# Kernel tuning notes

Measured on AMD Instinct MI355X. Metric: run time of the kernel, lower is better.

The kernel has to match this reference:

```python
import jax, jax.numpy as jnp
import numpy as np

KNB = 64  # max_num_neighbors in torch_geometric radius query


def fps(p, n):
    # Farthest point sampling, deterministic start at index 0. p: [N,3] -> [n] int32
    N = p.shape[0]
    def step(carry, _):
        d, last = carry
        d = jnp.minimum(d, jnp.sum((p - p[last]) ** 2, -1))
        return (d, jnp.argmax(d).astype(jnp.int32)), last
    _, idx = jax.lax.scan(step, (jnp.full((N,), jnp.inf, p.dtype), jnp.int32(0)), None, length=n)
    return idx


def mlp3(h, w1, b1, w2, b2, w3, b3):
    # torch_geometric-style MLP: Lin+ReLU per layer (batch_norm disabled)
    h = jax.nn.relu(h @ w1 + b1)
    h = jax.nn.relu(h @ w2 + b2)
    return jax.nn.relu(h @ w3 + b3)


def sa_module(x, pos, S, r, params):
    # PointNet++ set abstraction: FPS -> ball query -> per-edge MLP -> max pool.
    # x: [B,N,C], pos: [B,N,3] -> ([B,S,Cout], [B,S,3])
    B, N, _ = pos.shape
    idx = jax.vmap(lambda p: fps(p, S))(pos)                           # [B,S]
    ctr = jnp.take_along_axis(pos, idx[:, :, None], 1)                 # [B,S,3]
    d2 = jnp.sum((ctr[:, :, None, :] - pos[:, None, :, :]) ** 2, -1)   # [B,S,N]
    mask = d2 <= r * r
    # first KNB in-radius points in index order (emulates radius() neighbor cap)
    score = jnp.where(mask, (N - jnp.arange(N, dtype=jnp.int32))[None, None, :], 0)
    vals, nb = jax.lax.top_k(score, KNB)                               # [B,S,KNB]
    valid = vals > 0
    flat = nb.reshape(B, S * KNB)
    xj = jnp.take_along_axis(x, flat[:, :, None], 1).reshape(B, S, KNB, -1)
    pj = jnp.take_along_axis(pos, flat[:, :, None], 1).reshape(B, S, KNB, 3)
    feat = jnp.concatenate([xj, pj - ctr[:, :, None, :]], -1)          # [B,S,KNB,C+3]
    h = mlp3(feat, *params)
    h = jnp.where(valid[..., None], h, -jnp.inf)
    return h.max(axis=2), ctr                                          # max-aggr over ball


def setup_inputs() -> dict:
    key = jax.random.key(0)
    ks = jax.random.split(key, 64)
    inp = {}
    inp["x"] = jax.random.normal(ks[0], (16, 2048, 9), jnp.float32)
    inp["pos"] = jax.random.uniform(ks[1], (16, 2048, 3), dtype=jnp.float32)
    i = 2
    for tag, c0, c1, c2, c3 in [("s1", 12, 64, 64, 128), ("s2", 131, 128, 128, 256),
                                 ("s3", 259, 256, 512, 1024), ("f", 1024, 512, 512, 256)]:
        for j, (ci, co) in enumerate([(c0, c1), (c1, c2), (c2, c3)], 1):
            inp[f"{tag}w{j}"] = jax.random.normal(ks[i], (ci, co), jnp.float32) / np.sqrt(ci); i += 1
            inp[f"{tag}b{j}"] = jnp.zeros((co,), jnp.float32)
    for j, (ci, co) in enumerate([(1024, 512), (512, 256), (256, 256), (256, 128), (128, 128)], 1):
        inp[f"l{j}w"] = jax.random.normal(ks[i], (ci, co), jnp.float32) / np.sqrt(ci); i += 1
        inp[f"l{j}b"] = jnp.zeros((co,), jnp.float32)
    return inp


def reference(x, pos,
              s1w1, s1b1, s1w2, s1b2, s1w3, s1b3,
              s2w1, s2b1, s2w2, s2b2, s2w3, s2b3,
              s3w1, s3b1, s3w2, s3b2, s3w3, s3b3,
              fw1, fb1, fw2, fb2, fw3, fb3,
              l1w, l1b, l2w, l2b, l3w, l3b, l4w, l4b, l5w, l5b):
    KP1 = 4  # K+1 frames per sample; B = n_batch*(K+1)
    x1, p1 = sa_module(x, pos, 1024, 0.2, (s1w1, s1b1, s1w2, s1b2, s1w3, s1b3))
    x2, p2 = sa_module(x1, p1, 256, 0.4, (s2w1, s2b1, s2w2, s2b2, s2w3, s2b3))
    # GlobalSAModule: MLP then global max pool over remaining points
    g = mlp3(jnp.concatenate([x2, p2], -1), s3w1, s3b1, s3w2, s3b2, s3w3, s3b3).max(axis=1)  # [B,1024]
    h = jax.nn.relu(g @ l1w + l1b)
    h = jax.nn.relu(h @ l2w + l2b)
    h = h @ l3w + l3b                       # [B,256]
    h = h.reshape(-1, KP1 * 256)            # [n_batch, 1024]
    h = mlp3(h, fw1, fb1, fw2, fb2, fw3, fb3)  # fusion_type == 0
    h = jax.nn.relu(h @ l4w + l4b)
    return h @ l5w + l5b                    # [n_batch, z_dim=128]
```

## Files before the change

kernel.cpp:

```cpp
#include <hip/hip_runtime.h>
#include <cstddef>

#define DEVINF __builtin_inff()

typedef __attribute__((ext_vector_type(8))) short bf16x8;
typedef __attribute__((ext_vector_type(4))) float f32x4;
typedef __attribute__((ext_vector_type(2))) float f32x2;

__device__ __forceinline__ unsigned short f2bf(float x) {
  unsigned u = __float_as_uint(x);
  return (unsigned short)((u + 0x7fff + ((u >> 16) & 1)) >> 16);
}
__device__ __forceinline__ float bf2f(unsigned short h) {
  return __uint_as_float(((unsigned)h) << 16);
}
__device__ __forceinline__ void split_bf(float x, unsigned short& hi, unsigned short& lo) {
  hi = f2bf(x);
  lo = f2bf(x - bf2f(hi));
}

#define FPS_RED_LEVEL(CTRL)                                                      \
  {                                                                              \
    int th = __builtin_amdgcn_update_dpp((int)hi, (int)hi, CTRL, 0xf, 0xf, false); \
    int tl = __builtin_amdgcn_update_dpp((int)lo, (int)lo, CTRL, 0xf, 0xf, false); \
    bool take = ((unsigned)th > hi) || (((unsigned)th == hi) && ((unsigned)tl > lo)); \
    hi = take ? (unsigned)th : hi;                                               \
    lo = take ? (unsigned)tl : lo;                                               \
  }

template <int PPLH, int NCH>
__device__ __forceinline__ unsigned long long fps_wave_step(
    f32x2* qx, f32x2* qy, f32x2* qz, f32x2* d, float lx, float ly, float lz,
    int lane, int ibase) {
#pragma clang fp contract(off)
  const int CH = PPLH / NCH;
  float bv[NCH];
  int bi[NCH];
#pragma unroll
  for (int c = 0; c < NCH; ++c) { bv[c] = -DEVINF; bi[c] = 0x7fffffff; }
  f32x2 lxv = {lx, lx}, lyv = {ly, ly}, lzv = {lz, lz};
#pragma unroll
  for (int h = 0; h < PPLH; ++h) {
    const int c = h / CH;
    f32x2 dx = qx[h] - lxv, dy = qy[h] - lyv, dz = qz[h] - lzv;
    f32x2 t0 = dx * dx, t1 = dy * dy, t2 = dz * dz;
    f32x2 d2 = (t0 + t1) + t2;
    f32x2 dn;
    dn.x = fminf(d[h].x, d2.x);
    dn.y = fminf(d[h].y, d2.y);
    d[h] = dn;
    int i0 = ibase + (2 * h) * 64 + lane;
    if (dn.x > bv[c]) { bv[c] = dn.x; bi[c] = i0; }
    if (dn.y > bv[c]) { bv[c] = dn.y; bi[c] = i0 + 64; }
  }
  unsigned hi, lo;
  if (NCH == 4) {
    unsigned h0 = __float_as_uint(bv[0]), l0 = ~(unsigned)bi[0];
    unsigned h1 = __float_as_uint(bv[1]), l1 = ~(unsigned)bi[1];
    unsigned h2 = __float_as_uint(bv[2]), l2 = ~(unsigned)bi[2];
    unsigned h3 = __float_as_uint(bv[3]), l3 = ~(unsigned)bi[3];
    bool t01 = (h1 > h0) || ((h1 == h0) && (l1 > l0));
    unsigned ha = t01 ? h1 : h0, la = t01 ? l1 : l0;
    bool t23 = (h3 > h2) || ((h3 == h2) && (l3 > l2));
    unsigned hb = t23 ? h3 : h2, lb = t23 ? l3 : l2;
    bool tab = (hb > ha) || ((hb == ha) && (lb > la));
    hi = tab ? hb : ha;
    lo = tab ? lb : la;
  } else {
    const int c1 = (NCH > 1) ? 1 : 0;
    unsigned h0 = __float_as_uint(bv[0]), l0 = ~(unsigned)bi[0];
    unsigned h1 = __float_as_uint(bv[c1]), l1 = ~(unsigned)bi[c1];
    bool t01 = (h1 > h0) || ((h1 == h0) && (l1 > l0));
    hi = t01 ? h1 : h0;
    lo = t01 ? l1 : l0;
  }
  FPS_RED_LEVEL(0x111)
  FPS_RED_LEVEL(0x112)
  FPS_RED_LEVEL(0x114)
  FPS_RED_LEVEL(0x118)
  FPS_RED_LEVEL(0x142)
  FPS_RED_LEVEL(0x143)
  return (((unsigned long long)hi) << 32) | lo;
}

struct PrepJobs {
  const float* src[9];
  unsigned short* hi[9];
  unsigned short* lo[9];
  int K[9], N[9], rl[9];
  int blk0[10];
};

__global__ __launch_bounds__(256, 1) void fps1_prep_kernel(
    const float* __restrict__ pos, float* __restrict__ p1, PrepJobs jb) {
#pragma clang fp contract(off)
  const int tid = threadIdx.x;
  if (blockIdx.x >= 16) {
    int blk = blockIdx.x - 16;
    int j = 0;
#pragma unroll
    for (int t = 1; t < 9; ++t)
      if (blk >= jb.blk0[t]) j = t;
    int idx = (blk - jb.blk0[j]) * 256 + tid;
    int rl = jb.rl[j], N = jb.N[j], K = jb.K[j];
    if (idx >= N * rl) return;
    int n = idx / rl, k = idx - n * rl;
    float v = (k < K) ? jb.src[j][(size_t)k * N + n] : 0.f;
    unsigned short h, l;
    split_bf(v, h, l);
    jb.hi[j][idx] = h;
    jb.lo[j][idx] = l;
    return;
  }
  const int b = blockIdx.x;
  const int w = tid >> 6, lane = tid & 63;
  __shared__ __align__(16) float4 p4[2048];
  __shared__ __align__(16) float4 carr[1024];
  __shared__ unsigned long long kv[2][4];
  f32x2 qx[4], qy[4], qz[4], d[4];
  const int ibase = w * 512;
#pragma unroll
  for (int h = 0; h < 4; ++h) {
    int i0 = ibase + (2 * h) * 64 + lane, i1 = i0 + 64;
    const float* a = pos + ((size_t)b * 2048 + i0) * 3;
    const float* c = pos + ((size_t)b * 2048 + i1) * 3;
    float x0 = a[0], y0 = a[1], z0 = a[2];
    float x1 = c[0], y1 = c[1], z1 = c[2];
    qx[h].x = x0; qx[h].y = x1;
    qy[h].x = y0; qy[h].y = y1;
    qz[h].x = z0; qz[h].y = z1;
    d[h].x = DEVINF; d[h].y = DEVINF;
    p4[i0] = float4{x0, y0, z0, 0.f};
    p4[i1] = float4{x1, y1, z1, 0.f};
  }
  __syncthreads();
  int last = 0;
  for (int s = 0; s < 1024; ++s) {
    float4 c4 = p4[last];
    if (tid == 0) carr[s] = c4;
    unsigned long long k =
        fps_wave_step<4, 4>(qx, qy, qz, d, c4.x, c4.y, c4.z, lane, ibase);
    if (lane == 63) kv[s & 1][w] = k;
    __syncthreads();
    unsigned long long k0 = kv[s & 1][0], k1 = kv[s & 1][1];
    unsigned long long k2 = kv[s & 1][2], k3 = kv[s & 1][3];
    unsigned long long ka = k0 > k1 ? k0 : k1;
    unsigned long long kb = k2 > k3 ? k2 : k3;
    unsigned long long kk = ka > kb ? ka : kb;
    last = (int)~(unsigned)kk;
  }
  for (int i = tid; i < 1024; i += 256) {
    float4 c = carr[i];
    p1[((size_t)b * 1024 + i) * 3 + 0] = c.x;
    p1[((size_t)b * 1024 + i) * 3 + 1] = c.y;
    p1[((size_t)b * 1024 + i) * 3 + 2] = c.z;
  }
}

template <int KS, int T>
__device__ __forceinline__ void mfma_allm(
    const unsigned short* __restrict__ inHi, const unsigned short* __restrict__ inLo,
    int sIn, const unsigned short* __restrict__ wHi,
    const unsigned short* __restrict__ wLo, int rl, const float* __restrict__ bias,
    int n0, int lane, f32x4 acc[4][T]) {
  const int col = lane & 15, quad = lane >> 4;
#pragma unroll
  for (int t = 0; t < T; ++t) {
    float bv = bias[n0 + t * 16 + col];
#pragma unroll
    for (int mt = 0; mt < 4; ++mt) {
      acc[mt][t].x = bv; acc[mt][t].y = bv; acc[mt][t].z = bv; acc[mt][t].w = bv;
    }
  }
  size_t b0 = (size_t)(n0 + col) * rl + quad * 8;
  bf16x8 bh = *(const bf16x8*)(wHi + b0);
  bf16x8 bl = *(const bf16x8*)(wLo + b0);
#pragma unroll 1
  for (int ks = 0; ks < KS; ++ks) {
    bf16x8 ah[4], al[4];
#pragma unroll
    for (int mt = 0; mt < 4; ++mt) {
      int aoff = (mt * 16 + col) * sIn + ks * 32 + quad * 8;
      ah[mt] = *(const bf16x8*)(inHi + aoff);
      al[mt] = *(const bf16x8*)(inLo + aoff);
    }
#pragma unroll
    for (int t = 0; t < T; ++t) {
      int nks = (t + 1 < T) ? ks : ks + 1;
      int nt = (t + 1 < T) ? t + 1 : 0;
      if (nks > KS - 1) nks = KS - 1;
      size_t nboff = (size_t)(n0 + nt * 16 + col) * rl + nks * 32 + quad * 8;
      bf16x8 nh = *(const bf16x8*)(wHi + nboff);
      bf16x8 nl = *(const bf16x8*)(wLo + nboff);
#pragma unroll
      for (int mt = 0; mt < 4; ++mt) {
        acc[mt][t] = __builtin_amdgcn_mfma_f32_16x16x32_bf16(ah[mt], bh, acc[mt][t], 0, 0, 0);
        acc[mt][t] = __builtin_amdgcn_mfma_f32_16x16x32_bf16(ah[mt], bl, acc[mt][t], 0, 0, 0);
        acc[mt][t] = __builtin_amdgcn_mfma_f32_16x16x32_bf16(al[mt], bh, acc[mt][t], 0, 0, 0);
      }
      bh = nh;
      bl = nl;
    }
  }
}

template <int T>
__device__ __forceinline__ void store_allm(const f32x4 acc[4][T], int n0,
                                           unsigned short* outHi,
                                           unsigned short* outLo, int sOut,
                                           int lane) {
  const int col = lane & 15, quad = lane >> 4;
#pragma unroll
  for (int mt = 0; mt < 4; ++mt)
#pragma unroll
    for (int t = 0; t < T; ++t)
#pragma unroll
      for (int r = 0; r < 4; ++r) {
        int edge = mt * 16 + quad * 4 + r;
        float v = fmaxf(acc[mt][t][r], 0.f);
        unsigned short h, l;
        split_bf(v, h, l);
        outHi[edge * sOut + n0 + t * 16 + col] = h;
        outLo[edge * sOut + n0 + t * 16 + col] = l;
      }
}

template <int T>
__device__ __forceinline__ void outpool_allm(const f32x4 acc[4][T], int n0,
                                             float* __restrict__ outp, int nvalid,
                                             int lane) {
  const int col = lane & 15, quad = lane >> 4;
#pragma unroll
  for (int t = 0; t < T; ++t) {
    float m = -DEVINF;
#pragma unroll
    for (int mt = 0; mt < 4; ++mt)
#pragma unroll
      for (int r = 0; r < 4; ++r) {
        int edge = mt * 16 + quad * 4 + r;
        float v = fmaxf(acc[mt][t][r], 0.f);
        if (edge >= nvalid) v = -DEVINF;
        m = fmaxf(m, v);
      }
    m = fmaxf(m, __shfl_xor(m, 16, 64));
    m = fmaxf(m, __shfl_xor(m, 32, 64));
    if (quad == 0) outp[n0 + t * 16 + col] = m;
  }
}

template <int KS, int T>
__device__ __forceinline__ void mfma_1m(
    const unsigned short* __restrict__ inHi, const unsigned short* __restrict__ inLo,
    int sIn, const unsigned short* __restrict__ wHi,
    const unsigned short* __restrict__ wLo, int rl, const float* __restrict__ bias,
    int n0, int lane, f32x4 acc[T]) {
  const int col = lane & 15, quad = lane >> 4;
#pragma unroll
  for (int t = 0; t < T; ++t) {
    float bv = bias[n0 + t * 16 + col];
    acc[t].x = bv; acc[t].y = bv; acc[t].z = bv; acc[t].w = bv;
  }
  size_t b0 = (size_t)(n0 + col) * rl + quad * 8;
  bf16x8 bh = *(const bf16x8*)(wHi + b0);
  bf16x8 bl = *(const bf16x8*)(wLo + b0);
#pragma unroll 1
  for (int ks = 0; ks < KS; ++ks) {
    int aoff = col * sIn + ks * 32 + quad * 8;
    bf16x8 ah = *(const bf16x8*)(inHi + aoff);
    bf16x8 al = *(const bf16x8*)(inLo + aoff);
#pragma unroll
    for (int t = 0; t < T; ++t) {
      int nks = (t + 1 < T) ? ks : ks + 1;
      int nt = (t + 1 < T) ? t + 1 : 0;
      if (nks > KS - 1) nks = KS - 1;
      size_t nboff = (size_t)(n0 + nt * 16 + col) * rl + nks * 32 + quad * 8;
      bf16x8 nh = *(const bf16x8*)(wHi + nboff);
      bf16x8 nl = *(const bf16x8*)(wLo + nboff);
      acc[t] = __builtin_amdgcn_mfma_f32_16x16x32_bf16(ah, bh, acc[t], 0, 0, 0);
      acc[t] = __builtin_amdgcn_mfma_f32_16x16x32_bf16(ah, bl, acc[t], 0, 0, 0);
      acc[t] = __builtin_amdgcn_mfma_f32_16x16x32_bf16(al, bh, acc[t], 0, 0, 0);
      bh = nh;
      bl = nl;
    }
  }
}

template <int T>
__device__ __forceinline__ void store_1m(const f32x4 acc[T], int n0,
                                         unsigned short* outHi,
                                         unsigned short* outLo, int sOut, int lane) {
  const int col = lane & 15, quad = lane >> 4;
#pragma unroll
  for (int t = 0; t < T; ++t)
#pragma unroll
    for (int r = 0; r < 4; ++r) {
      int p = quad * 4 + r;
      float v = fmaxf(acc[t][r], 0.f);
      unsigned short h, l;
      split_bf(v, h, l);
      outHi[p * sOut + n0 + t * 16 + col] = h;
      outLo[p * sOut + n0 + t * 16 + col] = l;
    }
}

__global__ __launch_bounds__(256, 4) void sa1_kernel(
    const float* __restrict__ x,
    const float* __restrict__ pos,
    const float* __restrict__ ctr,
    float* __restrict__ p2,
    const unsigned short* __restrict__ w1h, const unsigned short* __restrict__ w1l,
    const unsigned short* __restrict__ w2h, const unsigned short* __restrict__ w2l,
    const unsigned short* __restrict__ w3h, const unsigned short* __restrict__ w3l,
    const float* __restrict__ b1, const float* __restrict__ b2,
    const float* __restrict__ b3,
    float* __restrict__ out)
{
  const int N = 2048;
  const float r2 = (float)(0.2 * 0.2);
  const int tid = threadIdx.x;
  const int w = tid >> 6, lane = tid & 63;
  __shared__ __align__(16) unsigned short smem[4 * 4608];
  unsigned short* bufA_hi = smem;
  unsigned short* bufA_lo = smem + 4608;
  unsigned short* bufB_hi = smem + 9216;
  unsigned short* bufB_lo = smem + 13824;
  __shared__ int nb[64];
  __shared__ int tot[4];
  __shared__ unsigned long long kv2[2][4];

  if (blockIdx.x < 16) {
    const int bb = blockIdx.x;
    float4* q4 = (float4*)smem;
    float4* carr = (float4*)(smem + 8192);
    for (int i = tid; i < 1024; i += 256) {
      const float* pr = ctr + ((size_t)bb * 1024 + i) * 3;
      q4[i] = float4{pr[0], pr[1], pr[2], 0.f};
    }
    __syncthreads();
    f32x2 qx[2], qy[2], qz[2], d[2];
    const int ibase = w * 256;
#pragma unroll
    for (int h = 0; h < 2; ++h) {
      int i0 = ibase + (2 * h) * 64 + lane, i1 = i0 + 64;
      float4 a = q4[i0], c = q4[i1];
      qx[h].x = a.x; qx[h].y = c.x;
      qy[h].x = a.y; qy[h].y = c.y;
      qz[h].x = a.z; qz[h].y = c.z;
      d[h].x = DEVINF; d[h].y = DEVINF;
    }
    int last = 0;
    for (int s = 0; s < 256; ++s) {
      float4 c4 = q4[last];
      if (tid == 0) carr[s] = c4;
      unsigned long long k =
          fps_wave_step<2, 2>(qx, qy, qz, d, c4.x, c4.y, c4.z, lane, ibase);
      if (lane == 63) kv2[s & 1][w] = k;
      __syncthreads();
      unsigned long long k0 = kv2[s & 1][0], k1 = kv2[s & 1][1];
      unsigned long long k2 = kv2[s & 1][2], k3 = kv2[s & 1][3];
      unsigned long long ka = k0 > k1 ? k0 : k1;
      unsigned long long kb = k2 > k3 ? k2 : k3;
      unsigned long long kk = ka > kb ? ka : kb;
      last = (int)~(unsigned)kk;
    }
    {
      float4 c = carr[tid];
      if (tid < 256) {
        p2[((size_t)bb * 256 + tid) * 3 + 0] = c.x;
        p2[((size_t)bb * 256 + tid) * 3 + 1] = c.y;
        p2[((size_t)bb * 256 + tid) * 3 + 2] = c.z;
      }
    }
    return;
  }

  const int bs = blockIdx.x - 16;
  const int b = bs >> 10;
  const float cx = ctr[bs * 3 + 0], cy = ctr[bs * 3 + 1], cz = ctr[bs * 3 + 2];
  nb[lane] = 0;
  unsigned long long mloc[8];
  {
#pragma clang fp contract(off)
#pragma unroll
    for (int it = 0; it < 8; ++it) {
      int i = (w * 8 + it) * 64 + lane;
      const float* p = pos + ((size_t)b * N + i) * 3;
      float dx = p[0] - cx, dy = p[1] - cy, dz = p[2] - cz;
      float t0 = dx * dx, t1 = dy * dy, t2 = dz * dz;
      float d2 = (t0 + t1) + t2;
      mloc[it] = __ballot(d2 <= r2);
    }
  }
  {
    int mytot = 0;
#pragma unroll
    for (int it = 0; it < 8; ++it) mytot += (int)__popcll(mloc[it]);
    if (lane == 0) tot[w] = mytot;
  }
  __syncthreads();
  const int t0s = tot[0], t1s = tot[1], t2s = tot[2], t3s = tot[3];
  {
    int cnt = (w > 0 ? t0s : 0) + (w > 1 ? t1s : 0) + (w > 2 ? t2s : 0);
#pragma unroll
    for (int it = 0; it < 8; ++it) {
      unsigned long long m = mloc[it];
      bool inr = (m >> lane) & 1;
      int posn = cnt + (int)__popcll(m & ((1ull << lane) - 1ull));
      if (inr && posn < 64) nb[posn] = (w * 8 + it) * 64 + lane;
      cnt += (int)__popcll(m);
    }
  }
  const int total = t0s + t1s + t2s + t3s;
  const int nvalid = total < 64 ? total : 64;
  __syncthreads();
  {
    int j = nb[lane];
    if (w < 3) {
      const float* xr = x + ((size_t)b * N + j) * 9 + w * 3;
      float f0 = xr[0], f1 = xr[1], f2 = xr[2];
      unsigned short h, l;
      split_bf(f0, h, l); bufA_hi[lane * 72 + w * 3 + 0] = h; bufA_lo[lane * 72 + w * 3 + 0] = l;
      split_bf(f1, h, l); bufA_hi[lane * 72 + w * 3 + 1] = h; bufA_lo[lane * 72 + w * 3 + 1] = l;
      split_bf(f2, h, l); bufA_hi[lane * 72 + w * 3 + 2] = h; bufA_lo[lane * 72 + w * 3 + 2] = l;
    } else {
      const float* pr = pos + ((size_t)b * N + j) * 3;
      float rr[3] = {pr[0] - cx, pr[1] - cy, pr[2] - cz};
#pragma unroll
      for (int c = 0; c < 3; ++c) {
        unsigned short h, l;
        split_bf(rr[c], h, l);
        bufA_hi[lane * 72 + 9 + c] = h;
        bufA_lo[lane * 72 + 9 + c] = l;
      }
#pragma unroll
      for (int k = 12; k < 32; ++k) {
        bufA_hi[lane * 72 + k] = 0;
        bufA_lo[lane * 72 + k] = 0;
      }
    }
  }
  __syncthreads();
  {
    f32x4 acc[4][1];
    mfma_allm<1, 1>(bufA_hi, bufA_lo, 72, w1h, w1l, 40, b1, w * 16, lane, acc);
    store_allm<1>(acc, w * 16, bufB_hi, bufB_lo, 72, lane);
  }
  __syncthreads();
  {
    f32x4 acc[4][1];
    mfma_allm<2, 1>(bufB_hi, bufB_lo, 72, w2h, w2l, 72, b2, w * 16, lane, acc);
    store_allm<1>(acc, w * 16, bufA_hi, bufA_lo, 72, lane);
  }
  __syncthreads();
  {
    f32x4 acc[4][2];
    mfma_allm<2, 2>(bufA_hi, bufA_lo, 72, w3h, w3l, 72, b3, w * 32, lane, acc);
    outpool_allm<2>(acc, w * 32, out + (size_t)bs * 128, nvalid, lane);
  }
}

__global__ __launch_bounds__(256, 2) void sa2_kernel(
    const float* __restrict__ x1,
    const float* __restrict__ pos1,
    const float* __restrict__ ctr,
    const unsigned short* __restrict__ w1h, const unsigned short* __restrict__ w1l,
    const unsigned short* __restrict__ w2h, const unsigned short* __restrict__ w2l,
    const unsigned short* __restrict__ w3h, const unsigned short* __restrict__ w3l,
    const float* __restrict__ b1, const float* __restrict__ b2,
    const float* __restrict__ b3,
    float* __restrict__ out)
{
  const int N = 1024;
  const float r2 = (float)(0.4 * 0.4);
  const int bs = blockIdx.x;
  const int b = bs >> 8;
  const int tid = threadIdx.x;
  const int w = tid >> 6, lane = tid & 63;
  const float cx = ctr[bs * 3 + 0], cy = ctr[bs * 3 + 1], cz = ctr[bs * 3 + 2];
  __shared__ __align__(16) unsigned short bufA_hi[64 * 168], bufA_lo[64 * 168];
  __shared__ __align__(16) unsigned short bufB_hi[64 * 136], bufB_lo[64 * 136];
  __shared__ int nb[64];
  __shared__ int tot[4];
  nb[lane] = 0;
  unsigned long long mloc[4];
  {
#pragma clang fp contract(off)
#pragma unroll
    for (int it = 0; it < 4; ++it) {
      int i = (w * 4 + it) * 64 + lane;
      const float* p = pos1 + ((size_t)b * N + i) * 3;
      float dx = p[0] - cx, dy = p[1] - cy, dz = p[2] - cz;
      float t0 = dx * dx, t1 = dy * dy, t2 = dz * dz;
      float d2 = (t0 + t1) + t2;
      mloc[it] = __ballot(d2 <= r2);
    }
  }
  {
    int mytot = 0;
#pragma unroll
    for (int it = 0; it < 4; ++it) mytot += (int)__popcll(mloc[it]);
    if (lane == 0) tot[w] = mytot;
  }
  __syncthreads();
  const int t0s = tot[0], t1s = tot[1], t2s = tot[2], t3s = tot[3];
  {
    int cnt = (w > 0 ? t0s : 0) + (w > 1 ? t1s : 0) + (w > 2 ? t2s : 0);
#pragma unroll
    for (int it = 0; it < 4; ++it) {
      unsigned long long m = mloc[it];
      bool inr = (m >> lane) & 1;
      int posn = cnt + (int)__popcll(m & ((1ull << lane) - 1ull));
      if (inr && posn < 64) nb[posn] = (w * 4 + it) * 64 + lane;
      cnt += (int)__popcll(m);
    }
  }
  const int total = t0s + t1s + t2s + t3s;
  const int nvalid = total < 64 ? total : 64;
  __syncthreads();
  {
    int j = nb[lane];
    const float* xr = x1 + ((size_t)b * N + j) * 128 + 32 * w;
#pragma unroll
    for (int g = 0; g < 8; ++g) {
      float4 v = *(const float4*)(xr + 4 * g);
      float vv[4] = {v.x, v.y, v.z, v.w};
#pragma unroll
      for (int e = 0; e < 4; ++e) {
        unsigned short h, l;
        split_bf(vv[e], h, l);
        int k = 32 * w + 4 * g + e;
        bufA_hi[lane * 168 + k] = h;
        bufA_lo[lane * 168 + k] = l;
      }
    }
    if (w == 0) {
      const float* pr = pos1 + ((size_t)b * N + j) * 3;
      float rr[3] = {pr[0] - cx, pr[1] - cy, pr[2] - cz};
#pragma unroll
      for (int c = 0; c < 3; ++c) {
        unsigned short h, l;
        split_bf(rr[c], h, l);
        bufA_hi[lane * 168 + 128 + c] = h;
        bufA_lo[lane * 168 + 128 + c] = l;
      }
#pragma unroll
      for (int k = 131; k < 160; ++k) {
        bufA_hi[lane * 168 + k] = 0;
        bufA_lo[lane * 168 + k] = 0;
      }
    }
  }
  __syncthreads();
  {
    f32x4 acc[4][2];
    mfma_allm<5, 2>(bufA_hi, bufA_lo, 168, w1h, w1l, 168, b1, w * 32, lane, acc);
    store_allm<2>(acc, w * 32, bufB_hi, bufB_lo, 136, lane);
  }
  __syncthreads();
  {
    f32x4 acc[4][2];
    mfma_allm<4, 2>(bufB_hi, bufB_lo, 136, w2h, w2l, 136, b2, w * 32, lane, acc);
    store_allm<2>(acc, w * 32, bufA_hi, bufA_lo, 168, lane);
  }
  __syncthreads();
  {
    f32x4 acc[4][4];
    mfma_allm<4, 4>(bufA_hi, bufA_lo, 168, w3h, w3l, 136, b3, w * 64, lane, acc);
    outpool_allm<4>(acc, w * 64, out + (size_t)bs * 256, nvalid, lane);
  }
}

__global__ __launch_bounds__(256, 2) void gsa_kernel(
    const float* __restrict__ x2,
    const float* __restrict__ p2,
    const unsigned short* __restrict__ g1h, const unsigned short* __restrict__ g1l,
    const unsigned short* __restrict__ g2h, const unsigned short* __restrict__ g2l,
    const unsigned short* __restrict__ g3h, const unsigned short* __restrict__ g3l,
    const float* __restrict__ b1, const float* __restrict__ b2,
    const float* __restrict__ b3,
    float* __restrict__ part)
{
  const int blk = blockIdx.x;
  const int bt = blk >> 4, gidx = blk & 15;
  const int tid = threadIdx.x;
  const int w = tid >> 6, lane = tid & 63;
  const int p0 = gidx * 16;
  __shared__ __align__(16) unsigned short inH[16 * 296], inL[16 * 296];
  __shared__ __align__(16) unsigned short h1H[16 * 264], h1L[16 * 264];
  __shared__ __align__(16) unsigned short h2H[16 * 520], h2L[16 * 520];
  {
    int p = tid >> 4, seg = tid & 15;
    const float* xr = x2 + ((size_t)(bt * 256 + p0 + p)) * 256 + seg * 16;
#pragma unroll
    for (int g = 0; g < 4; ++g) {
      float4 v = *(const float4*)(xr + 4 * g);
      float vv[4] = {v.x, v.y, v.z, v.w};
#pragma unroll
      for (int e = 0; e < 4; ++e) {
        unsigned short h, l;
        split_bf(vv[e], h, l);
        int k = seg * 16 + 4 * g + e;
        inH[p * 296 + k] = h;
        inL[p * 296 + k] = l;
      }
    }
    if (tid < 16) {
      const float* pr = p2 + (bt * 256 + p0 + tid) * 3;
#pragma unroll
      for (int c = 0; c < 3; ++c) {
        unsigned short h, l;
        split_bf(pr[c], h, l);
        inH[tid * 296 + 256 + c] = h;
        inL[tid * 296 + 256 + c] = l;
      }
      for (int k = 259; k < 288; ++k) {
        inH[tid * 296 + k] = 0;
        inL[tid * 296 + k] = 0;
      }
    }
  }
  __syncthreads();
  {
    f32x4 acc[4];
    mfma_1m<9, 4>(inH, inL, 296, g1h, g1l, 296, b1, w * 64, lane, acc);
    store_1m<4>(acc, w * 64, h1H, h1L, 264, lane);
  }
  __syncthreads();
  {
    f32x4 acc[8];
    mfma_1m<8, 8>(h1H, h1L, 264, g2h, g2l, 264, b2, w * 128, lane, acc);
    store_1m<8>(acc, w * 128, h2H, h2L, 520, lane);
  }
  __syncthreads();
  {
    f32x4 acc[16];
    mfma_1m<16, 16>(h2H, h2L, 520, g3h, g3l, 520, b3, w * 256, lane, acc);
    const int col = lane & 15;
    float* op = part + ((size_t)(bt * 16 + gidx)) * 1024 + w * 256;
#pragma unroll
    for (int t = 0; t < 16; ++t) {
      float m = -DEVINF;
#pragma unroll
      for (int r = 0; r < 4; ++r) m = fmaxf(m, fmaxf(acc[t][r], 0.f));
      m = fmaxf(m, __shfl_xor(m, 16, 64));
      m = fmaxf(m, __shfl_xor(m, 32, 64));
      if ((lane >> 4) == 0) op[t * 16 + col] = m;
    }
  }
}

__global__ __launch_bounds__(256) void head1_kernel(
    const float* __restrict__ part,
    const float* __restrict__ l1w, const float* __restrict__ l1b,
    const float* __restrict__ l2w, const float* __restrict__ l2b,
    const float* __restrict__ l3w, const float* __restrict__ l3b,
    float* __restrict__ hC)
{
  const int m = blockIdx.x;
  const int tid = threadIdx.x;
  __shared__ float gA[1024];
  __shared__ float hX[512];
  __shared__ float hY[256];
#pragma unroll
  for (int j = 0; j < 4; ++j) {
    int c = j * 256 + tid;
    float mx = -DEVINF;
#pragma unroll
    for (int t = 0; t < 16; ++t)
      mx = fmaxf(mx, part[((size_t)(m * 16 + t)) * 1024 + c]);
    gA[c] = mx;
  }
  __syncthreads();
  {
    float a0 = l1b[tid], a1 = l1b[tid + 256];
#pragma unroll 4
    for (int k = 0; k < 1024; ++k) {
      float v = gA[k];
      a0 = fmaf(v, l1w[(size_t)k * 512 + tid], a0);
      a1 = fmaf(v, l1w[(size_t)k * 512 + tid + 256], a1);
    }
    hX[tid] = fmaxf(a0, 0.f);
    hX[tid + 256] = fmaxf(a1, 0.f);
  }
  __syncthreads();
  {
    float a = l2b[tid];
#pragma unroll 4
    for (int k = 0; k < 512; ++k) a = fmaf(hX[k], l2w[(size_t)k * 256 + tid], a);
    hY[tid] = fmaxf(a, 0.f);
  }
  __syncthreads();
  {
    float a = l3b[tid];
#pragma unroll 4
    for (int k = 0; k < 256; ++k) a = fmaf(hY[k], l3w[(size_t)k * 256 + tid], a);
    hC[(size_t)m * 256 + tid] = a;
  }
}

__global__ __launch_bounds__(256) void head2_kernel(
    const float* __restrict__ hC,
    const float* __restrict__ fw1, const float* __restrict__ fb1,
    const float* __restrict__ fw2, const float* __restrict__ fb2,
    const float* __restrict__ fw3, const float* __restrict__ fb3,
    const float* __restrict__ l4w, const float* __restrict__ l4b,
    const float* __restrict__ l5w, const float* __restrict__ l5b,
    float* __restrict__ out)
{
  const int m = blockIdx.x;
  const int tid = threadIdx.x;
  __shared__ float A[1024];
  __shared__ float Bf[512];
#pragma unroll
  for (int j = 0; j < 4; ++j) A[j * 256 + tid] = hC[(size_t)m * 1024 + j * 256 + tid];
  __syncthreads();
  {
    float a0 = fb1[tid], a1 = fb1[tid + 256];
#pragma unroll 4
    for (int k = 0; k < 1024; ++k) {
      float v = A[k];
      a0 = fmaf(v, fw1[(size_t)k * 512 + tid], a0);
      a1 = fmaf(v, fw1[(size_t)k * 512 + tid + 256], a1);
    }
    Bf[tid] = fmaxf(a0, 0.f);
    Bf[tid + 256] = fmaxf(a1, 0.f);
  }
  __syncthreads();
  {
    float a0 = fb2[tid], a1 = fb2[tid + 256];
#pragma unroll 4
    for (int k = 0; k < 512; ++k) {
      float v = Bf[k];
      a0 = fmaf(v, fw2[(size_t)k * 512 + tid], a0);
      a1 = fmaf(v, fw2[(size_t)k * 512 + tid + 256], a1);
    }
    __syncthreads();
    A[tid] = fmaxf(a0, 0.f);
    A[tid + 256] = fmaxf(a1, 0.f);
  }
  __syncthreads();
  {
    float a = fb3[tid];
#pragma unroll 4
    for (int k = 0; k < 512; ++k) a = fmaf(A[k], fw3[(size_t)k * 256 + tid], a);
    __syncthreads();
    Bf[tid] = fmaxf(a, 0.f);
  }
  __syncthreads();
  {
    if (tid < 128) {
      float a = l4b[tid];
#pragma unroll 4
      for (int k = 0; k < 256; ++k) a = fmaf(Bf[k], l4w[(size_t)k * 128 + tid], a);
      A[tid] = fmaxf(a, 0.f);
    }
  }
  __syncthreads();
  {
    if (tid < 128) {
      float a = l5b[tid];
#pragma unroll 4
      for (int k = 0; k < 128; ++k) a = fmaf(A[k], l5w[(size_t)k * 128 + tid], a);
      out[(size_t)m * 128 + tid] = a;
    }
  }
}

extern "C" void kernel_launch(void* const* d_in, const int* in_sizes, int n_in,
                              void* d_out, int out_size, void* d_ws, size_t ws_size,
                              hipStream_t stream) {
  (void)in_sizes; (void)n_in; (void)out_size; (void)ws_size;
  const float* x    = (const float*)d_in[0];
  const float* pos  = (const float*)d_in[1];
  const float* s1w1 = (const float*)d_in[2];  const float* s1b1 = (const float*)d_in[3];
  const float* s1w2 = (const float*)d_in[4];  const float* s1b2 = (const float*)d_in[5];
  const float* s1w3 = (const float*)d_in[6];  const float* s1b3 = (const float*)d_in[7];
  const float* s2w1 = (const float*)d_in[8];  const float* s2b1 = (const float*)d_in[9];
  const float* s2w2 = (const float*)d_in[10]; const float* s2b2 = (const float*)d_in[11];
  const float* s2w3 = (const float*)d_in[12]; const float* s2b3 = (const float*)d_in[13];
  const float* s3w1 = (const float*)d_in[14]; const float* s3b1 = (const float*)d_in[15];
  const float* s3w2 = (const float*)d_in[16]; const float* s3b2 = (const float*)d_in[17];
  const float* s3w3 = (const float*)d_in[18]; const float* s3b3 = (const float*)d_in[19];
  const float* fw1  = (const float*)d_in[20]; const float* fb1  = (const float*)d_in[21];
  const float* fw2  = (const float*)d_in[22]; const float* fb2  = (const float*)d_in[23];
  const float* fw3  = (const float*)d_in[24]; const float* fb3  = (const float*)d_in[25];
  const float* l1w  = (const float*)d_in[26]; const float* l1b  = (const float*)d_in[27];
  const float* l2w  = (const float*)d_in[28]; const float* l2b  = (const float*)d_in[29];
  const float* l3w  = (const float*)d_in[30]; const float* l3b  = (const float*)d_in[31];
  const float* l4w  = (const float*)d_in[32]; const float* l4b  = (const float*)d_in[33];
  const float* l5w  = (const float*)d_in[34]; const float* l5b  = (const float*)d_in[35];
  float* out = (float*)d_out;

  float* ws = (float*)d_ws;
  float* p1   = ws;
  float* x1   = p1 + 49152;
  float* p2   = x1 + 2097152;
  float* x2   = p2 + 12288;
  float* part = x2 + 1048576;
  float* hC   = part + 262144;
  unsigned short* wp = (unsigned short*)(hC + 4096);
  unsigned short* s1w1h = wp;              unsigned short* s1w1l = s1w1h + 2560;
  unsigned short* s1w2h = s1w1l + 2560;    unsigned short* s1w2l = s1w2h + 4608;
  unsigned short* s1w3h = s1w2l + 4608;    unsigned short* s1w3l = s1w3h + 9216;
  unsigned short* s2w1h = s1w3l + 9216;    unsigned short* s2w1l = s2w1h + 21504;
  unsigned short* s2w2h = s2w1l + 21504;   unsigned short* s2w2l = s2w2h + 17408;
  unsigned short* s2w3h = s2w2l + 17408;   unsigned short* s2w3l = s2w3h + 34816;
  unsigned short* g1h   = s2w3l + 34816;   unsigned short* g1l   = g1h + 75776;
  unsigned short* g2h   = g1l + 75776;     unsigned short* g2l   = g2h + 135168;
  unsigned short* g3h   = g2l + 135168;    unsigned short* g3l   = g3h + 532480;

  PrepJobs jb;
  const float* srcs[9] = {s1w1, s1w2, s1w3, s2w1, s2w2, s2w3, s3w1, s3w2, s3w3};
  unsigned short* his[9] = {s1w1h, s1w2h, s1w3h, s2w1h, s2w2h, s2w3h, g1h, g2h, g3h};
  unsigned short* los[9] = {s1w1l, s1w2l, s1w3l, s2w1l, s2w2l, s2w3l, g1l, g2l, g3l};
  int Ks[9]  = {12, 64, 64, 131, 128, 128, 259, 256, 512};
  int Ns[9]  = {64, 64, 128, 128, 128, 256, 256, 512, 1024};
  int rls[9] = {40, 72, 72, 168, 136, 136, 296, 264, 520};
  int acc_blk = 0;
  for (int j = 0; j < 9; ++j) {
    jb.src[j] = srcs[j]; jb.hi[j] = his[j]; jb.lo[j] = los[j];
    jb.K[j] = Ks[j]; jb.N[j] = Ns[j]; jb.rl[j] = rls[j];
    jb.blk0[j] = acc_blk;
    acc_blk += (Ns[j] * rls[j] + 255) / 256;
  }
  jb.blk0[9] = acc_blk;

  fps1_prep_kernel<<<16 + acc_blk, 256, 0, stream>>>(pos, p1, jb);
  sa1_kernel<<<16 * 1024 + 16, 256, 0, stream>>>(x, pos, p1, p2, s1w1h, s1w1l,
                                                 s1w2h, s1w2l, s1w3h, s1w3l,
                                                 s1b1, s1b2, s1b3, x1);
  sa2_kernel<<<16 * 256, 256, 0, stream>>>(x1, p1, p2, s2w1h, s2w1l, s2w2h,
                                           s2w2l, s2w3h, s2w3l, s2b1, s2b2,
                                           s2b3, x2);
  gsa_kernel<<<256, 256, 0, stream>>>(x2, p2, g1h, g1l, g2h, g2l, g3h, g3l,
                                      s3b1, s3b2, s3b3, part);
  head1_kernel<<<16, 256, 0, stream>>>(part, l1w, l1b, l2w, l2b, l3w, l3b, hC);
  head2_kernel<<<4, 256, 0, stream>>>(hC, fw1, fb1, fw2, fb2, fw3, fb3, l4w,
                                      l4b, l5w, l5b, out);
}
```

Before: 1.401 ms.

## Run first-stage FPS in a single wavefront to remove block barriers

The first farthest-point-sampling stage now runs on one 64-lane wave per batch element. Each lane holds 32 points in registers, and the argmax is reduced entirely with DPP and readlane, so the per-step __syncthreads and shared-memory key exchange across four waves are gone. Centroids are written straight to global memory each step instead of being staged in shared memory and copied out at the end. The trade-off is four times more serial arithmetic per lane per step and more register pressure, in exchange for removing 1024 block-wide barriers.

After: 1.642 ms. 1.17x slower.

```diff
diff --git a/kernel.cpp b/kernel.cpp
--- a/kernel.cpp
+++ b/kernel.cpp
@@ -27,6 +27,55 @@
     hi = take ? (unsigned)th : hi;                                               \
     lo = take ? (unsigned)tl : lo;                                               \
   }
+
+#define FPS_DECL_H(h) f32x2 qx##h, qy##h, qz##h, dd##h;
+
+#define FPS_GLOAD_H(h)                                                           \
+  {                                                                              \
+    int vi0 = (h)*128 + lane;                                                    \
+    const float* va = gpos + (size_t)vi0 * 3;                                    \
+    const float* vc = gpos + (size_t)(vi0 + 64) * 3;                             \
+    float vx0 = va[0], vy0 = va[1], vz0 = va[2];                                 \
+    float vx1 = vc[0], vy1 = vc[1], vz1 = vc[2];                                 \
+    qx##h.x = vx0; qx##h.y = vx1;                                                \
+    qy##h.x = vy0; qy##h.y = vy1;                                                \
+    qz##h.x = vz0; qz##h.y = vz1;                                                \
+    dd##h.x = DEVINF; dd##h.y = DEVINF;                                          \
+    p4[vi0] = float4{vx0, vy0, vz0, 0.f};                                        \
+    p4[vi0 + 64] = float4{vx1, vy1, vz1, 0.f};                                   \
+  }
+
+#define FPS_UPD_H(h, c)                                                          \
+  {                                                                              \
+    f32x2 vdx = qx##h - lxv, vdy = qy##h - lyv, vdz = qz##h - lzv;               \
+    f32x2 vt0 = vdx * vdx, vt1 = vdy * vdy, vt2 = vdz * vdz;                     \
+    f32x2 vsq = (vt0 + vt1) + vt2;                                               \
+    f32x2 vdn;                                                                   \
+    vdn.x = fminf(dd##h.x, vsq.x);                                               \
+    vdn.y = fminf(dd##h.y, vsq.y);                                               \
+    dd##h = vdn;                                                                 \
+    if (vdn.x > bv##c) { bv##c = vdn.x; bi##c = (h)*128; }                       \
+    if (vdn.y > bv##c) { bv##c = vdn.y; bi##c = (h)*128 + 64; }                  \
+  }
+
+#define FPS_KEY_MERGE4(wl)                                                       \
+  unsigned h0 = __float_as_uint(bv0), l0 = ~(unsigned)(bi0 + (wl));              \
+  unsigned h1 = __float_as_uint(bv1), l1 = ~(unsigned)(bi1 + (wl));              \
+  unsigned h2 = __float_as_uint(bv2), l2 = ~(unsigned)(bi2 + (wl));              \
+  unsigned h3 = __float_as_uint(bv3), l3 = ~(unsigned)(bi3 + (wl));              \
+  bool t01 = (h1 > h0) || ((h1 == h0) && (l1 > l0));                             \
+  unsigned ha = t01 ? h1 : h0, la = t01 ? l1 : l0;                               \
+  bool t23 = (h3 > h2) || ((h3 == h2) && (l3 > l2));                             \
+  unsigned hb = t23 ? h3 : h2, lb = t23 ? l3 : l2;                               \
+  bool tab = (hb > ha) || ((hb == ha) && (lb > la));                             \
+  unsigned hi = tab ? hb : ha;                                                   \
+  unsigned lo = tab ? lb : la;                                                   \
+  FPS_RED_LEVEL(0x111)                                                           \
+  FPS_RED_LEVEL(0x112)                                                           \
+  FPS_RED_LEVEL(0x114)                                                           \
+  FPS_RED_LEVEL(0x118)                                                           \
+  FPS_RED_LEVEL(0x142)                                                           \
+  FPS_RED_LEVEL(0x143)
 
 template <int PPLH, int NCH>
 __device__ __forceinline__ unsigned long long fps_wave_step(
@@ -54,19 +103,7 @@
     if (dn.y > bv[c]) { bv[c] = dn.y; bi[c] = i0 + 64; }
   }
   unsigned hi, lo;
-  if (NCH == 4) {
-    unsigned h0 = __float_as_uint(bv[0]), l0 = ~(unsigned)bi[0];
-    unsigned h1 = __float_as_uint(bv[1]), l1 = ~(unsigned)bi[1];
-    unsigned h2 = __float_as_uint(bv[2]), l2 = ~(unsigned)bi[2];
-    unsigned h3 = __float_as_uint(bv[3]), l3 = ~(unsigned)bi[3];
-    bool t01 = (h1 > h0) || ((h1 == h0) && (l1 > l0));
-    unsigned ha = t01 ? h1 : h0, la = t01 ? l1 : l0;
-    bool t23 = (h3 > h2) || ((h3 == h2) && (l3 > l2));
-    unsigned hb = t23 ? h3 : h2, lb = t23 ? l3 : l2;
-    bool tab = (hb > ha) || ((hb == ha) && (lb > la));
-    hi = tab ? hb : ha;
-    lo = tab ? lb : la;
-  } else {
+  {
     const int c1 = (NCH > 1) ? 1 : 0;
     unsigned h0 = __float_as_uint(bv[0]), l0 = ~(unsigned)bi[0];
     unsigned h1 = __float_as_uint(bv[c1]), l1 = ~(unsigned)bi[c1];
@@ -113,47 +150,41 @@
     return;
   }
   const int b = blockIdx.x;
-  const int w = tid >> 6, lane = tid & 63;
+  if (tid >= 64) return;
+  const int lane = tid;
   __shared__ __align__(16) float4 p4[2048];
-  __shared__ __align__(16) float4 carr[1024];
-  __shared__ unsigned long long kv[2][4];
-  f32x2 qx[4], qy[4], qz[4], d[4];
-  const int ibase = w * 512;
-#pragma unroll
-  for (int h = 0; h < 4; ++h) {
-    int i0 = ibase + (2 * h) * 64 + lane, i1 = i0 + 64;
-    const float* a = pos + ((size_t)b * 2048 + i0) * 3;
-    const float* c = pos + ((size_t)b * 2048 + i1) * 3;
-    float x0 = a[0], y0 = a[1], z0 = a[2];
-    float x1 = c[0], y1 = c[1], z1 = c[2];
-    qx[h].x = x0; qx[h].y = x1;
-    qy[h].x = y0; qy[h].y = y1;
-    qz[h].x = z0; qz[h].y = z1;
-    d[h].x = DEVINF; d[h].y = DEVINF;
-    p4[i0] = float4{x0, y0, z0, 0.f};
-    p4[i1] = float4{x1, y1, z1, 0.f};
-  }
-  __syncthreads();
-  int last = 0;
+  const float* gpos = pos + (size_t)b * 2048 * 3;
+  FPS_DECL_H(0) FPS_DECL_H(1) FPS_DECL_H(2) FPS_DECL_H(3)
+  FPS_DECL_H(4) FPS_DECL_H(5) FPS_DECL_H(6) FPS_DECL_H(7)
+  FPS_DECL_H(8) FPS_DECL_H(9) FPS_DECL_H(10) FPS_DECL_H(11)
+  FPS_DECL_H(12) FPS_DECL_H(13) FPS_DECL_H(14) FPS_DECL_H(15)
+  FPS_GLOAD_H(0) FPS_GLOAD_H(1) FPS_GLOAD_H(2) FPS_GLOAD_H(3)
+  FPS_GLOAD_H(4) FPS_GLOAD_H(5) FPS_GLOAD_H(6) FPS_GLOAD_H(7)
+  FPS_GLOAD_H(8) FPS_GLOAD_H(9) FPS_GLOAD_H(10) FPS_GLOAD_H(11)
+  FPS_GLOAD_H(12) FPS_GLOAD_H(13) FPS_GLOAD_H(14) FPS_GLOAD_H(15)
+  float cx = __uint_as_float((unsigned)__builtin_amdgcn_readlane((int)__float_as_uint(qx0.x), 0));
+  float cy = __uint_as_float((unsigned)__builtin_amdgcn_readlane((int)__float_as_uint(qy0.x), 0));
+  float cz = __uint_as_float((unsigned)__builtin_amdgcn_readlane((int)__float_as_uint(qz0.x), 0));
+  float* p1b = p1 + (size_t)b * 1024 * 3;
   for (int s = 0; s < 1024; ++s) {
+    if (lane == 0) {
+      p1b[3 * s + 0] = cx;
+      p1b[3 * s + 1] = cy;
+      p1b[3 * s + 2] = cz;
+    }
+    if (s == 1023) break;
+    f32x2 lxv = {cx, cx}, lyv = {cy, cy}, lzv = {cz, cz};
+    float bv0 = -DEVINF, bv1 = -DEVINF, bv2 = -DEVINF, bv3 = -DEVINF;
+    int bi0 = 0, bi1 = 0, bi2 = 0, bi3 = 0;
+    FPS_UPD_H(0, 0) FPS_UPD_H(1, 0) FPS_UPD_H(2, 0) FPS_UPD_H(3, 0)
+    FPS_UPD_H(4, 1) FPS_UPD_H(5, 1) FPS_UPD_H(6, 1) FPS_UPD_H(7, 1)
+    FPS_UPD_H(8, 2) FPS_UPD_H(9, 2) FPS_UPD_H(10, 2) FPS_UPD_H(11, 2)
+    FPS_UPD_H(12, 3) FPS_UPD_H(13, 3) FPS_UPD_H(14, 3) FPS_UPD_H(15, 3)
+    FPS_KEY_MERGE4(lane)
+    unsigned wlo = (unsigned)__builtin_amdgcn_readlane((int)lo, 63);
+    int last = (int)~wlo;
     float4 c4 = p4[last];
-    if (tid == 0) carr[s] = c4;
-    unsigned long long k =
-        fps_wave_step<4, 4>(qx, qy, qz, d, c4.x, c4.y, c4.z, lane, ibase);
-    if (lane == 63) kv[s & 1][w] = k;
-    __syncthreads();
-    unsigned long long k0 = kv[s & 1][0], k1 = kv[s & 1][1];
-    unsigned long long k2 = kv[s & 1][2], k3 = kv[s & 1][3];
-    unsigned long long ka = k0 > k1 ? k0 : k1;
-    unsigned long long kb = k2 > k3 ? k2 : k3;
-    unsigned long long kk = ka > kb ? ka : kb;
-    last = (int)~(unsigned)kk;
-  }
-  for (int i = tid; i < 1024; i += 256) {
-    float4 c = carr[i];
-    p1[((size_t)b * 1024 + i) * 3 + 0] = c.x;
-    p1[((size_t)b * 1024 + i) * 3 + 1] = c.y;
-    p1[((size_t)b * 1024 + i) * 3 + 2] = c.z;
+    cx = c4.x; cy = c4.y; cz = c4.z;
   }
 }
 
```
